# Performance work log

Measured on AMD Instinct MI355X. Metric: run time of the kernel, lower is better.

Reference implementation:

```python
import jax, jax.numpy as jnp
import numpy as np


def setup_inputs() -> dict:
    key = jax.random.key(0)
    k1, k2, k3, k4 = jax.random.split(key, 4)
    N, E, F, H = 100000, 1600000, 128, 128
    x = jax.random.normal(k1, (N, F), dtype=jnp.float32)
    edge_index = jax.random.randint(k2, (2, E), 0, N, dtype=jnp.int64)
    W1 = jax.random.normal(k3, (F, H), dtype=jnp.float32) * (1.0 / np.sqrt(F))
    b1 = jnp.zeros((H,), dtype=jnp.float32)
    W2 = jax.random.normal(k4, (H, H), dtype=jnp.float32) * (1.0 / np.sqrt(H))
    b2 = jnp.zeros((H,), dtype=jnp.float32)
    return {"x": x, "edge_index": edge_index, "W1": W1, "b1": b1, "W2": W2, "b2": b2}


def reference(x, edge_index, W1, b1, W2, b2):
    # Two-layer cached GCN: norm is computed once (cached) and reused by both layers.
    N = x.shape[0]
    loops = jnp.arange(N, dtype=edge_index.dtype)
    src = jnp.concatenate([edge_index[0], loops])  # add self-loops
    dst = jnp.concatenate([edge_index[1], loops])
    # symmetric GCN normalization: deg^-1/2[src] * deg^-1/2[dst]
    deg = jax.ops.segment_sum(jnp.ones_like(dst, dtype=x.dtype), dst, num_segments=N)
    dinv = jnp.where(deg > 0, jax.lax.rsqrt(deg), 0.0)
    norm = dinv[src] * dinv[dst]  # [E+N]

    def conv(h, W, b):
        h = h @ W  # dense transform before sparse aggregate (cheaper: out_dim small)
        msg = norm[:, None] * h[src]  # gather + scale
        return jax.ops.segment_sum(msg, dst, num_segments=N) + b

    h = jax.nn.relu(conv(x, W1, b1))
    # dropout is identity in eval mode (deterministic reference)
    return conv(h, W2, b2)
```

## Files before the change

### kernel.cpp

```cpp
#include <hip/hip_runtime.h>


#define BKT_SHIFT 7
#define BKT_NODES 128
#define CH 8192
#define MAXBKT 1024

typedef _Float16 half4v __attribute__((ext_vector_type(4)));
typedef _Float16 half8v __attribute__((ext_vector_type(8)));
typedef float float4v __attribute__((ext_vector_type(4)));

__global__ __launch_bounds__(256) void k_prep(const float* __restrict__ W1,
                                              const float* __restrict__ W2,
                                              _Float16* __restrict__ wt1,
                                              _Float16* __restrict__ wt2,
                                              int* __restrict__ bcnt,
                                              int* __restrict__ dcnt, int nbkt) {
    int i = blockIdx.x * 256 + threadIdx.x;
    if (i < 16384) {
        int k = i >> 7, c = i & 127;
        wt1[c * 128 + k] = (_Float16)W1[i];
    } else {
        int j = i - 16384;
        int k = j >> 7, c = j & 127;
        wt2[c * 128 + k] = (_Float16)W2[j];
    }
    if (i < nbkt) bcnt[i] = 0;
    if (i < 2) dcnt[i] = 0;
}

__global__ __launch_bounds__(256) void k_bincount_scan(const int* __restrict__ dst,
                                                       int* __restrict__ bcnt,
                                                       int* __restrict__ bofs,
                                                       int* __restrict__ bcur,
                                                       int* __restrict__ dcnt,
                                                       int E, int nbkt, int nblocks) {
    __shared__ int sh[MAXBKT];
    const int t = threadIdx.x;
    for (int i = t; i < nbkt; i += 256) sh[i] = 0;
    __syncthreads();
    for (long long e = (long long)blockIdx.x * 256 + t; e < E;
         e += (long long)nblocks * 256)
        atomicAdd(&sh[dst[e] >> BKT_SHIFT], 1);
    __syncthreads();
    for (int i = t; i < nbkt; i += 256)
        if (sh[i]) atomicAdd(&bcnt[i], sh[i]);
    __threadfence();
    __syncthreads();
    __shared__ int last;
    if (t == 0) last = (atomicAdd(&dcnt[0], 1) == nblocks - 1);
    __syncthreads();
    if (!last) return;
    __threadfence();
    int v[4];
    int s = 0;
    for (int k = 0; k < 4; k++) {
        int idx = t * 4 + k;
        v[k] = (idx < nbkt) ? atomicAdd(&bcnt[idx], 0) : 0;
        s += v[k];
    }
    __syncthreads();
    int x = s;
    sh[t] = x;
    __syncthreads();
    for (int o = 1; o < 256; o <<= 1) {
        int y = (t >= o) ? sh[t - o] : 0;
        __syncthreads();
        x += y;
        sh[t] = x;
        __syncthreads();
    }
    int run = x - s;
    for (int k = 0; k < 4; k++) {
        int idx = t * 4 + k;
        if (idx < nbkt) { bofs[idx] = run; bcur[idx] = run; }
        run += v[k];
    }
    if (t == 0) bofs[nbkt] = E;
}

__global__ __launch_bounds__(256) void k_binfill(const int* __restrict__ src,
                                                 const int* __restrict__ dst,
                                                 int* __restrict__ bcur,
                                                 unsigned* __restrict__ recs,
                                                 int E, int nbkt) {
    __shared__ unsigned stage[CH];
    __shared__ unsigned short stageb[CH];
    __shared__ int cnt[MAXBKT];
    __shared__ int base[MAXBKT];
    const int t = threadIdx.x;
    const long long c0 = (long long)blockIdx.x * CH;

    for (int i = t; i < nbkt; i += 256) cnt[i] = 0;
    __syncthreads();

    for (int k = 0; k < CH / 256; k++) {
        int i = k * 256 + t;
        long long e = c0 + i;
        if (e < E) {
            int d = dst[e];
            int b = d >> BKT_SHIFT;
            stage[i] = ((unsigned)(d & (BKT_NODES - 1)) << 17) | (unsigned)src[e];
            stageb[i] = (unsigned short)b;
            atomicAdd(&cnt[b], 1);
        }
    }
    __syncthreads();

    for (int i = t; i < nbkt; i += 256) {
        int c = cnt[i];
        base[i] = c ? atomicAdd(&bcur[i], c) : 0;
        cnt[i] = 0;
    }
    __syncthreads();

    for (int k = 0; k < CH / 256; k++) {
        int i = k * 256 + t;
        if (c0 + i < E) {
            int b = stageb[i];
            int p = base[b] + atomicAdd(&cnt[b], 1);
            recs[p] = stage[i];
        }
    }
}

__global__ __launch_bounds__(256) void k_fill_all(const unsigned* __restrict__ recs,
                                                  const int* __restrict__ bofs,
                                                  float* __restrict__ dinv,
                                                  int* __restrict__ ofs,
                                                  int* __restrict__ col,
                                                  int n, int E) {
    __shared__ int cnt[BKT_NODES];
    __shared__ int sc[BKT_NODES];
    const int b = blockIdx.x, t = threadIdx.x;
    const int beg = bofs[b], end = bofs[b + 1];

    if (t < BKT_NODES) cnt[t] = 0;
    __syncthreads();
    for (int j = beg + t; j < end; j += 256)
        atomicAdd(&cnt[recs[j] >> 17], 1);
    __syncthreads();

    int v = 0, x = 0;
    if (t < BKT_NODES) { v = cnt[t]; x = v; sc[t] = x; }
    __syncthreads();
    for (int o = 1; o < BKT_NODES; o <<= 1) {
        int y = (t >= o && t < BKT_NODES) ? sc[t - o] : 0;
        __syncthreads();
        if (t < BKT_NODES) { x += y; sc[t] = x; }
        __syncthreads();
    }

    const int d0 = b << BKT_SHIFT;
    if (t < BKT_NODES) {
        int off = beg + x - v;
        int node = d0 + t;
        if (node < n) {
            ofs[node] = off;
            dinv[node] = rsqrtf((float)v + 1.0f);
        }
        cnt[t] = off;
    }
    if (b == 0 && t == 0) ofs[n] = E;
    __syncthreads();

    for (int j = beg + t; j < end; j += 256) {
        unsigned r = recs[j];
        int p = atomicAdd(&cnt[r >> 17], 1);
        col[p] = (int)(r & 0x1FFFF);
    }
}

template <int IN_HALF>
__global__ __launch_bounds__(256, 4) void k_gemm_mfma(const void* __restrict__ inp,
                                                      const _Float16* __restrict__ Wt,
                                                      const float* __restrict__ dinv,
                                                      _Float16* __restrict__ out, int n) {
    __shared__ _Float16 Bl[128][136];
    const int t = threadIdx.x;
    const int row0 = blockIdx.x * 64;

    for (int i = t; i < 128 * 16; i += 256) {
        int r = i >> 4, c8 = i & 15;
        *(half8v*)&Bl[r][c8 * 8] = *(const half8v*)&Wt[r * 128 + c8 * 8];
    }
    __syncthreads();

    const int wave = t >> 6;
    const int lane = t & 63;
    const int m0 = wave * 16;
    const int ml = lane & 15;
    const int quad = lane >> 4;

    int r = row0 + m0 + ml;
    if (r >= n) r = n - 1;

    float4v acc[8] = {};
#pragma unroll
    for (int kc = 0; kc < 4; kc++) {
        half8v a;
        if (IN_HALF) {
            a = *(const half8v*)((const _Float16*)inp + (size_t)r * 128 + kc * 32 + quad * 8);
        } else {
            const float* ap = (const float*)inp + (size_t)r * 128 + kc * 32 + quad * 8;
            float4v v0 = *(const float4v*)ap;
            float4v v1 = *(const float4v*)(ap + 4);
#pragma unroll
            for (int k = 0; k < 4; k++) {
                a[k] = (_Float16)v0[k];
                a[4 + k] = (_Float16)v1[k];
            }
        }
#pragma unroll
        for (int nt = 0; nt < 8; nt++) {
            half8v bfr = *(const half8v*)&Bl[nt * 16 + ml][kc * 32 + quad * 8];
            acc[nt] = __builtin_amdgcn_mfma_f32_16x16x32_f16(a, bfr, acc[nt], 0, 0, 0);
        }
    }

    int nr = n - row0;
    if (nr > 64) nr = 64;
#pragma unroll
    for (int reg = 0; reg < 4; reg++) {
        int rr = m0 + quad * 4 + reg;
        if (rr < nr) {
            float dv = dinv[row0 + rr];
#pragma unroll
            for (int nt = 0; nt < 8; nt++)
                out[(size_t)(row0 + rr) * 128 + nt * 16 + ml] =
                    (_Float16)(acc[nt][reg] * dv);
        }
    }
}

template <int OUT_HALF>
__global__ __launch_bounds__(256) void k_agg_csr(const int* __restrict__ ofs,
                                                 const int* __restrict__ col,
                                                 const float* __restrict__ dinv,
                                                 const half4v* __restrict__ ts,
                                                 const float* __restrict__ bias,
                                                 void* __restrict__ outp, int n) {
    int gid = blockIdx.x * 256 + threadIdx.x;
    int row = gid >> 5;
    int lane = gid & 31;
    if (row >= n) return;

    float dd = dinv[row];
    int beg = ofs[row];
    int end = ofs[row + 1];

    half4v sv = ts[(size_t)row * 32 + lane];
    float4 acc = make_float4((float)sv[0], (float)sv[1], (float)sv[2], (float)sv[3]);

    int j = beg;
    for (; j + 3 < end; j += 4) {
        int s0 = col[j], s1 = col[j + 1], s2 = col[j + 2], s3 = col[j + 3];
        half4v v0 = ts[(size_t)s0 * 32 + lane];
        half4v v1 = ts[(size_t)s1 * 32 + lane];
        half4v v2 = ts[(size_t)s2 * 32 + lane];
        half4v v3 = ts[(size_t)s3 * 32 + lane];
        acc.x += (float)v0[0] + (float)v1[0] + (float)v2[0] + (float)v3[0];
        acc.y += (float)v0[1] + (float)v1[1] + (float)v2[1] + (float)v3[1];
        acc.z += (float)v0[2] + (float)v1[2] + (float)v2[2] + (float)v3[2];
        acc.w += (float)v0[3] + (float)v1[3] + (float)v2[3] + (float)v3[3];
    }
    for (; j < end; j++) {
        half4v v = ts[(size_t)col[j] * 32 + lane];
        acc.x += (float)v[0];
        acc.y += (float)v[1];
        acc.z += (float)v[2];
        acc.w += (float)v[3];
    }

    float4 bv = *(const float4*)&bias[lane * 4];
    if (OUT_HALF) {
        half4v hv;
        hv[0] = (_Float16)fmaxf(bv.x + dd * acc.x, 0.f);
        hv[1] = (_Float16)fmaxf(bv.y + dd * acc.y, 0.f);
        hv[2] = (_Float16)fmaxf(bv.z + dd * acc.z, 0.f);
        hv[3] = (_Float16)fmaxf(bv.w + dd * acc.w, 0.f);
        ((half4v*)outp)[(size_t)row * 32 + lane] = hv;
    } else {
        float4 o;
        o.x = bv.x + dd * acc.x;
        o.y = bv.y + dd * acc.y;
        o.z = bv.z + dd * acc.z;
        o.w = bv.w + dd * acc.w;
        *(float4*)&((float*)outp)[(size_t)row * 128 + lane * 4] = o;
    }
}

extern "C" void kernel_launch(void* const* d_in, const int* in_sizes, int n_in,
                              void* d_out, int out_size, void* d_ws, size_t ws_size,
                              hipStream_t stream) {
    const int N = in_sizes[0] / 128;
    const int E = in_sizes[1] / 2;
    const float* x  = (const float*)d_in[0];
    const int*   ei = (const int*)d_in[1];
    const float* W1 = (const float*)d_in[2];
    const float* b1 = (const float*)d_in[3];
    const float* W2 = (const float*)d_in[4];
    const float* b2 = (const float*)d_in[5];

    const int* src = ei;
    const int* dst = ei + E;

    const int NBKT = (N + BKT_NODES - 1) / BKT_NODES;

    _Float16* t    = (_Float16*)d_ws;
    _Float16* wt1  = t + (size_t)N * 128;
    _Float16* wt2  = wt1 + 16384;
    float*    dinv = (float*)(wt2 + 16384);
    int*      ofs  = (int*)(dinv + N);
    unsigned* recs = (unsigned*)(ofs + ((N + 2 + 255) & ~255));
    int*      col  = (int*)(recs + E);
    int*      bofs = col + E;
    int*      bcur = bofs + NBKT + 1;
    int*      bcnt = bcur + NBKT;
    int*      dcnt = bcnt + NBKT;

    _Float16* h16 = (_Float16*)d_out;
    float*    out = (float*)d_out;

    const int nb_g = (N + 63) / 64;
    const int nb_a = (int)(((long long)N * 32 + 255) / 256);
    const int nb_c = (int)(((long long)E + CH - 1) / CH);

    k_prep<<<128, 256, 0, stream>>>(W1, W2, wt1, wt2, bcnt, dcnt, NBKT);
    k_bincount_scan<<<256, 256, 0, stream>>>(dst, bcnt, bofs, bcur, dcnt, E, NBKT, 256);
    k_binfill<<<nb_c, 256, 0, stream>>>(src, dst, bcur, recs, E, NBKT);
    k_fill_all<<<NBKT, 256, 0, stream>>>(recs, bofs, dinv, ofs, col, N, E);

    k_gemm_mfma<0><<<nb_g, 256, 0, stream>>>(x, wt1, dinv, t, N);
    k_agg_csr<1><<<nb_a, 256, 0, stream>>>(ofs, col, dinv, (const half4v*)t, b1, h16, N);

    k_gemm_mfma<1><<<nb_g, 256, 0, stream>>>(h16, wt2, dinv, t, N);
    k_agg_csr<0><<<nb_a, 256, 0, stream>>>(ofs, col, dinv, (const half4v*)t, b2, out, N);
}
```

Measured before the change: 328.1 us.

## Store transformed features in column-sliced layout and aggregate per slice

The GEMM now writes its fp16 output as 8 column slices of 16 features each, every slice a contiguous [N x 16] array, instead of row-major [N x 128]. The aggregation kernel assigns each block one slice and 128 rows, with two threads per row each gathering 8 halfs. The aim is for each slice's working set (about 3.2 MB) to fit in cache, so random neighbour gathers hit L2 or MALL rather than HBM. The cost is eight passes over the CSR index arrays, narrower 32-byte gathers, and strided GEMM stores; final outputs also switch to nontemporal stores.

```diff
diff --git a/kernel.cpp b/kernel.cpp
--- a/kernel.cpp
+++ b/kernel.cpp
@@ -175,7 +175,7 @@
 __global__ __launch_bounds__(256, 4) void k_gemm_mfma(const void* __restrict__ inp,
                                                       const _Float16* __restrict__ Wt,
                                                       const float* __restrict__ dinv,
-                                                      _Float16* __restrict__ out, int n) {
+                                                      _Float16* __restrict__ tsb, int n) {
     __shared__ _Float16 Bl[128][136];
     const int t = threadIdx.x;
     const int row0 = blockIdx.x * 64;
@@ -227,66 +227,78 @@
             float dv = dinv[row0 + rr];
 #pragma unroll
             for (int nt = 0; nt < 8; nt++)
-                out[(size_t)(row0 + rr) * 128 + nt * 16 + ml] =
+                tsb[(size_t)nt * n * 16 + (size_t)(row0 + rr) * 16 + ml] =
                     (_Float16)(acc[nt][reg] * dv);
         }
     }
 }
 
 template <int OUT_HALF>
-__global__ __launch_bounds__(256) void k_agg_csr(const int* __restrict__ ofs,
-                                                 const int* __restrict__ col,
-                                                 const float* __restrict__ dinv,
-                                                 const half4v* __restrict__ ts,
-                                                 const float* __restrict__ bias,
-                                                 void* __restrict__ outp, int n) {
-    int gid = blockIdx.x * 256 + threadIdx.x;
-    int row = gid >> 5;
-    int lane = gid & 31;
+__global__ __launch_bounds__(256) void k_agg_slice(const int* __restrict__ ofs,
+                                                   const int* __restrict__ col,
+                                                   const float* __restrict__ dinv,
+                                                   const _Float16* __restrict__ tsb,
+                                                   const float* __restrict__ bias,
+                                                   void* __restrict__ outp, int n) {
+    const int blk = blockIdx.x;
+    const int slice = blk & 7;
+    const int chunk = blk >> 3;
+    const int t = threadIdx.x;
+    const int row = chunk * 128 + (t >> 1);
     if (row >= n) return;
+    const int half = t & 1;
+    const int c0 = slice * 16 + half * 8;
+    const _Float16* base = tsb + (size_t)slice * n * 16 + half * 8;
 
     float dd = dinv[row];
     int beg = ofs[row];
     int end = ofs[row + 1];
 
-    half4v sv = ts[(size_t)row * 32 + lane];
-    float4 acc = make_float4((float)sv[0], (float)sv[1], (float)sv[2], (float)sv[3]);
+    half8v sv = *(const half8v*)(base + (size_t)row * 16);
+    float acc[8];
+#pragma unroll
+    for (int k = 0; k < 8; k++) acc[k] = (float)sv[k];
 
     int j = beg;
     for (; j + 3 < end; j += 4) {
         int s0 = col[j], s1 = col[j + 1], s2 = col[j + 2], s3 = col[j + 3];
-        half4v v0 = ts[(size_t)s0 * 32 + lane];
-        half4v v1 = ts[(size_t)s1 * 32 + lane];
-        half4v v2 = ts[(size_t)s2 * 32 + lane];
-        half4v v3 = ts[(size_t)s3 * 32 + lane];
-        acc.x += (float)v0[0] + (float)v1[0] + (float)v2[0] + (float)v3[0];
-        acc.y += (float)v0[1] + (float)v1[1] + (float)v2[1] + (float)v3[1];
-        acc.z += (float)v0[2] + (float)v1[2] + (float)v2[2] + (float)v3[2];
-        acc.w += (float)v0[3] + (float)v1[3] + (float)v2[3] + (float)v3[3];
+        half8v v0 = *(const half8v*)(base + (size_t)s0 * 16);
+        half8v v1 = *(const half8v*)(base + (size_t)s1 * 16);
+        half8v v2 = *(const half8v*)(base + (size_t)s2 * 16);
+        half8v v3 = *(const half8v*)(base + (size_t)s3 * 16);
+#pragma unroll
+        for (int k = 0; k < 8; k++)
+            acc[k] += (float)v0[k] + (float)v1[k] + (float)v2[k] + (float)v3[k];
     }
     for (; j < end; j++) {
-        half4v v = ts[(size_t)col[j] * 32 + lane];
-        acc.x += (float)v[0];
-        acc.y += (float)v[1];
-        acc.z += (float)v[2];
-        acc.w += (float)v[3];
-    }
-
-    float4 bv = *(const float4*)&bias[lane * 4];
+        int s = col[j];
+        half8v v = *(const half8v*)(base + (size_t)s * 16);
+#pragma unroll
+        for (int k = 0; k < 8; k++) acc[k] += (float)v[k];
+    }
+
+    float4v bv0 = *(const float4v*)&bias[c0];
+    float4v bv1 = *(const float4v*)&bias[c0 + 4];
+
     if (OUT_HALF) {
-        half4v hv;
-        hv[0] = (_Float16)fmaxf(bv.x + dd * acc.x, 0.f);
-        hv[1] = (_Float16)fmaxf(bv.y + dd * acc.y, 0.f);
-        hv[2] = (_Float16)fmaxf(bv.z + dd * acc.z, 0.f);
-        hv[3] = (_Float16)fmaxf(bv.w + dd * acc.w, 0.f);
-        ((half4v*)outp)[(size_t)row * 32 + lane] = hv;
+        half8v hv;
+#pragma unroll
+        for (int k = 0; k < 4; k++) {
+            hv[k] = (_Float16)fmaxf(bv0[k] + dd * acc[k], 0.f);
+            hv[4 + k] = (_Float16)fmaxf(bv1[k] + dd * acc[4 + k], 0.f);
+        }
+        __builtin_nontemporal_store(hv,
+            (half8v*)((_Float16*)outp + (size_t)row * 128 + c0));
     } else {
-        float4 o;
-        o.x = bv.x + dd * acc.x;
-        o.y = bv.y + dd * acc.y;
-        o.z = bv.z + dd * acc.z;
-        o.w = bv.w + dd * acc.w;
-        *(float4*)&((float*)outp)[(size_t)row * 128 + lane * 4] = o;
+        float4v o0, o1;
+#pragma unroll
+        for (int k = 0; k < 4; k++) {
+            o0[k] = bv0[k] + dd * acc[k];
+            o1[k] = bv1[k] + dd * acc[4 + k];
+        }
+        float* op = (float*)outp + (size_t)row * 128 + c0;
+        __builtin_nontemporal_store(o0, (float4v*)op);
+        __builtin_nontemporal_store(o1, (float4v*)(op + 4));
     }
 }
 
@@ -323,7 +335,7 @@
     float*    out = (float*)d_out;
 
     const int nb_g = (N + 63) / 64;
-    const int nb_a = (int)(((long long)N * 32 + 255) / 256);
+    const int nb_a = ((N + 127) / 128) * 8;
     const int nb_c = (int)(((long long)E + CH - 1) / CH);
 
     k_prep<<<128, 256, 0, stream>>>(W1, W2, wt1, wt2, bcnt, dcnt, NBKT);
@@ -332,8 +344,8 @@
     k_fill_all<<<NBKT, 256, 0, stream>>>(recs, bofs, dinv, ofs, col, N, E);
 
     k_gemm_mfma<0><<<nb_g, 256, 0, stream>>>(x, wt1, dinv, t, N);
-    k_agg_csr<1><<<nb_a, 256, 0, stream>>>(ofs, col, dinv, (const half4v*)t, b1, h16, N);
+    k_agg_slice<1><<<nb_a, 256, 0, stream>>>(ofs, col, dinv, t, b1, h16, N);
 
     k_gemm_mfma<1><<<nb_g, 256, 0, stream>>>(h16, wt2, dinv, t, N);
-    k_agg_csr<0><<<nb_a, 256, 0, stream>>>(ofs, col, dinv, (const half4v*)t, b2, out, N);
-}
+    k_agg_slice<0><<<nb_a, 256, 0, stream>>>(ofs, col, dinv, t, b2, out, N);
+}
```

Result: slower. 388.0 us (+18.3%).
